# Kernel tuning notes

Hardware: AMD Instinct MI355X
Metric: run time of the kernel (lower is better)

## Reference

```python
import math
import jax, jax.numpy as jnp
import numpy as np

C = 256          # channels
HID = 64         # max(int(C*0.25),16)
RH = 64          # max(C//4,32) router hidden
N, S, H, W = 8, 64, 16, 16
LOW_FREQ_RATIO = 0.2
ROUTER_TEMP = 1.0
LN_EPS = 1e-5

def gelu(v):
    return jax.nn.gelu(v, approximate=False)

def bn1d(v, s, b):  # folded eval-mode BatchNorm1d: (N,C,S)
    return v * s[None, :, None] + b[None, :, None]

def conv1x1(v, w, b=None):  # v:(N,Cin,S), w:(Cout,Cin)
    o = jnp.einsum('oc,ncs->nos', w, v)
    if b is not None:
        o = o + b[None, :, None]
    return o

def convk(v, w):  # v:(N,Cin,S), w:(Cout,Cin,K), 'same' padding
    k = w.shape[-1]
    return jax.lax.conv_general_dilated(v, w, (1,), [(k // 2, k // 2)],
                                        dimension_numbers=('NCH', 'OIH', 'NCH'))

def setup_inputs():
    key = jax.random.key(0)
    ks = iter(jax.random.split(key, 64))
    def nrm(shape, sc=0.02):
        return jax.random.normal(next(ks), shape, jnp.float32) * sc
    d = {}
    d['x'] = jax.random.normal(next(ks), (N, C, S, H, W), jnp.float32)
    d['ln_g'] = jnp.ones((C,), jnp.float32)
    d['ln_b'] = jnp.zeros((C,), jnp.float32)
    for k in (3, 5, 7):
        d['mb_w%d' % k] = nrm((C, 3 * C, k))
        d['mb_s%d' % k] = 1.0 + nrm((C,))
        d['mb_b%d' % k] = nrm((C,))
    d['mf_w'] = nrm((C, C)); d['mf_s'] = 1.0 + nrm((C,)); d['mf_b'] = nrm((C,))
    d['pg_w1'] = nrm((HID, 3)); d['pg_s1'] = 1.0 + nrm((HID,)); d['pg_b1'] = nrm((HID,))
    d['pg_w2'] = nrm((C, HID)); d['pg_b2'] = nrm((C,))
    d['pp_w'] = nrm((C, C)); d['pp_s'] = 1.0 + nrm((C,)); d['pp_b'] = nrm((C,))
    d['mg_w'] = nrm((C, 2 * C)); d['mg_b'] = nrm((C,))
    d['mo_w1'] = nrm((C, 3 * C)); d['mo_s1'] = 1.0 + nrm((C,)); d['mo_b1'] = nrm((C,))
    d['mo_w2'] = nrm((C, C))
    d['rt_w1'] = nrm((RH, C + 5)); d['rt_b1'] = nrm((RH,))
    d['rt_w2'] = nrm((3, RH)); d['rt_b2'] = nrm((3,))
    d['bp_w1'] = nrm((C, 4 * C)); d['bp_s1'] = 1.0 + nrm((C,)); d['bp_b1'] = nrm((C,))
    d['bp_w2'] = nrm((C, C))
    d['res_scale'] = jnp.full((1, C, 1), 0.05, jnp.float32)
    d['fg_w'] = nrm((C, C)); d['fg_b'] = nrm((C,))
    d['sg_w'] = nrm((C, C)); d['sg_s'] = 1.0 + nrm((C,)); d['sg_b'] = nrm((C,))
    return d

def _forward(x, ln_g, ln_b, mb_w3, mb_s3, mb_b3, mb_w5, mb_s5, mb_b5,
             mb_w7, mb_s7, mb_b7, mf_w, mf_s, mf_b,
             pg_w1, pg_s1, pg_b1, pg_w2, pg_b2, pp_w, pp_s, pp_b,
             mg_w, mg_b, mo_w1, mo_s1, mo_b1, mo_w2,
             rt_w1, rt_b1, rt_w2, rt_b2, bp_w1, bp_s1, bp_b1, bp_w2,
             res_scale, fg_w, fg_b, sg_w, sg_s, sg_b):
    n, c, s = x.shape[:3]
    x32 = x.astype(jnp.float32)
    desc = x32.mean(axis=(-1, -2))                     # (N,C,S)
    t = desc.transpose(0, 2, 1)                        # (N,S,C)
    mu = t.mean(-1, keepdims=True)
    var = t.var(-1, keepdims=True)
    dn = (((t - mu) / jnp.sqrt(var + LN_EPS)) * ln_g + ln_b).transpose(0, 2, 1)  # (N,C,S)

    def tdiff(v, order):
        dd = v[:, :, order:] - v[:, :, :-order]
        return jnp.pad(dd, ((0, 0), (0, 0), (order, 0)))
    diff1 = tdiff(dn, 1)
    diff2 = tdiff(dn, 2)

    # motion branch (multi-kernel conv1d + BN + GELU)
    mi = jnp.concatenate([dn, diff1, diff2], axis=1)   # (N,3C,S)
    motion = 0.0
    for w, bs, bb in ((mb_w3, mb_s3, mb_b3), (mb_w5, mb_s5, mb_b5), (mb_w7, mb_s7, mb_b7)):
        motion = motion + gelu(bn1d(convk(mi, w), bs, bb))
    motion = gelu(bn1d(conv1x1(motion / 3.0, mf_w), mf_s, mf_b))

    # FFT-based cycle / phase estimation
    tokens = dn.transpose(0, 2, 1)                     # (N,S,C)
    freq = jnp.fft.rfft(tokens, axis=1, norm='ortho')  # (N,F,C) complex
    fe = jnp.abs(freq).mean(-1)                        # (N,F)
    Fb = fe.shape[1]
    low = min(max(int(round(Fb * LOW_FREQ_RATIO)), 1), Fb - 1)
    he = fe[:, low:]
    peak_rel = jnp.argmax(he, axis=-1)                 # (N,)
    peak_idx = peak_rel + low
    peak_val = jnp.take_along_axis(he, peak_rel[:, None], axis=1)
    cycle_conf = peak_val / jnp.maximum(he.sum(axis=1, keepdims=True), 1e-6)  # (N,1)
    peak_norm = peak_idx.astype(jnp.float32)[:, None] / float(Fb - 1)
    mean_freq = freq.mean(-1)                          # (N,F) complex
    dom = jnp.take_along_axis(mean_freq, peak_idx[:, None], axis=1)[:, 0]
    dom_phase = jnp.arctan2(dom.imag, dom.real)
    tax = jnp.arange(s, dtype=jnp.float32)
    ang = (2.0 * math.pi / max(s, 1)) * peak_idx.astype(jnp.float32)
    arg = ang[:, None] * tax[None, :] + dom_phase[:, None]
    phase_cos = jnp.cos(arg)[:, None, :]               # (N,1,S)
    phase_sin = jnp.sin(arg)[:, None, :]

    cycle_token = jnp.broadcast_to(cycle_conf[:, :, None], (n, 1, s))
    pf = jnp.concatenate([phase_cos, phase_sin, cycle_token], axis=1)  # (N,3,S)
    pgate = jax.nn.sigmoid(conv1x1(gelu(bn1d(conv1x1(pf, pg_w1), pg_s1, pg_b1)), pg_w2, pg_b2))
    phase = gelu(bn1d(conv1x1(dn * pgate, pp_w), pp_s, pp_b))

    # bidirectional EMA memory via lax.scan
    gate = jax.nn.sigmoid(conv1x1(jnp.concatenate([dn, jnp.abs(diff1)], axis=1), mg_w, mg_b))
    g = gate.transpose(2, 0, 1)                        # (S,N,C)
    dd = dn.transpose(2, 0, 1)
    def step(st, gd):
        gt, dt = gd
        st = gt * st + (1.0 - gt) * dt
        return st, st
    _, fo = jax.lax.scan(step, dd[0], (g[1:], dd[1:]))
    fwd_mem = jnp.concatenate([dd[:1], fo], axis=0).transpose(1, 2, 0)
    _, bo = jax.lax.scan(step, dd[-1], (g[-2::-1], dd[-2::-1]))
    bwd_mem = jnp.concatenate([dd[-1:], bo], axis=0)[::-1].transpose(1, 2, 0)
    memory = conv1x1(gelu(bn1d(conv1x1(
        jnp.concatenate([dn, fwd_mem, bwd_mem], axis=1), mo_w1), mo_s1, mo_b1)), mo_w2)

    # router
    seq_std = dn.std(axis=2).mean(axis=1, keepdims=True)
    diff_energy = jnp.abs(diff1).mean(axis=(1, 2))[:, None]
    motion_energy = jnp.abs(motion).mean(axis=(1, 2))[:, None]
    memory_energy = jnp.abs(memory - dn).mean(axis=(1, 2))[:, None]
    stats = jnp.concatenate([seq_std, diff_energy, cycle_conf, peak_norm,
                             memory_energy + motion_energy], axis=-1)
    ri = jnp.concatenate([dn.mean(-1), stats], axis=-1)  # (N,C+5)
    hdn = gelu(ri @ rt_w1.T + rt_b1)
    logits = hdn @ rt_w2.T + rt_b2
    bw = jax.nn.softmax(logits / max(ROUTER_TEMP, 1e-6), axis=-1)  # (N,3)
    fused = (bw[:, 0, None, None] * motion + bw[:, 1, None, None] * phase
             + bw[:, 2, None, None] * memory)

    delta = conv1x1(gelu(bn1d(conv1x1(
        jnp.concatenate([dn, fused, motion - phase, memory - dn], axis=1),
        bp_w1), bp_s1, bp_b1)), bp_w2)
    delta = delta * jax.nn.sigmoid(conv1x1(dn, fg_w, fg_b))
    delta = res_scale * delta
    delta = delta[:, :, :, None, None]                 # (N,C,S,1,1)

    sp = x32.mean(axis=2)                              # (N,C,H,W)
    sg_lin = jnp.einsum('oc,nchw->nohw', sg_w, sp)
    sgate = jax.nn.sigmoid(sg_lin * sg_s[None, :, None, None] + sg_b[None, :, None, None])
    delta = delta * sgate[:, :, None, :, :]            # (N,C,S,H,W)
    return x + delta.astype(x.dtype)

def reference(x, ln_g, ln_b, mb_w3, mb_s3, mb_b3, mb_w5, mb_s5, mb_b5,
              mb_w7, mb_s7, mb_b7, mf_w, mf_s, mf_b,
              pg_w1, pg_s1, pg_b1, pg_w2, pg_b2, pp_w, pp_s, pp_b,
              mg_w, mg_b, mo_w1, mo_s1, mo_b1, mo_w2,
              rt_w1, rt_b1, rt_w2, rt_b2, bp_w1, bp_s1, bp_b1, bp_w2,
              res_scale, fg_w, fg_b, sg_w, sg_s, sg_b):
    return _forward(x, ln_g, ln_b, mb_w3, mb_s3, mb_b3, mb_w5, mb_s5, mb_b5,
                    mb_w7, mb_s7, mb_b7, mf_w, mf_s, mf_b,
                    pg_w1, pg_s1, pg_b1, pg_w2, pg_b2, pp_w, pp_s, pp_b,
                    mg_w, mg_b, mo_w1, mo_s1, mo_b1, mo_w2,
                    rt_w1, rt_b1, rt_w2, rt_b2, bp_w1, bp_s1, bp_b1, bp_w2,
                    res_scale, fg_w, fg_b, sg_w, sg_s, sg_b)
```

## Files before the change

kernel.cpp:

```cpp
#include <hip/hip_runtime.h>
#include <math.h>

namespace {

constexpr int N_ = 8, C_ = 256, S_ = 64, HW_ = 256;
constexpr int NS = N_ * S_;
constexpr int NHW = N_ * HW_;

constexpr size_t O_DESC  = 0;
constexpr size_t O_DN    = 131072;
constexpr size_t O_MOT   = 393216;
constexpr size_t O_GATE  = 524288;
constexpr size_t O_MEM   = 786432;
constexpr size_t O_PHASE = 1048576;
constexpr size_t O_DELTA = 1441792;
constexpr size_t O_SCN   = 1572864;
constexpr size_t O_SPT   = 2752512;
constexpr size_t O_SGATE = 3276800;
constexpr size_t O_FE    = 3801088;
constexpr size_t O_MFRE  = 3801600;
constexpr size_t O_MFIM  = 3802112;
constexpr size_t O_BW    = 3802656;
constexpr size_t O_ATMF  = 3802688;
constexpr size_t O_ATMG  = 3868224;
constexpr size_t O_ATMO1 = 3999296;
constexpr size_t O_ATMO2 = 4195904;
constexpr size_t O_ATPP  = 4261440;
constexpr size_t O_ATBP1 = 4326976;
constexpr size_t O_ATBP2 = 4589120;
constexpr size_t O_ATFG  = 4654656;
constexpr size_t O_ATSG  = 4720192;
constexpr size_t O_WFRAG = 4785728;
constexpr size_t O_IM2   = 6850112;
constexpr size_t O_CONVC = 8226368;

typedef __attribute__((ext_vector_type(4))) float f32x4;
typedef __attribute__((ext_vector_type(8))) short s16x8;
typedef __attribute__((ext_vector_type(8))) unsigned short u16x8;

__device__ __forceinline__ float gelu_f(float v) {
  return 0.5f * v * (1.0f + erff(v * 0.70710678118654752f));
}
__device__ __forceinline__ float sigmoid_f(float v) {
  return 1.0f / (1.0f + expf(-v));
}
__device__ __forceinline__ unsigned short f2bf(float f) {
  unsigned int u = __float_as_uint(f);
  u += 0x7fffu + ((u >> 16) & 1u);
  return (unsigned short)(u >> 16);
}

__device__ __forceinline__ float block_sum256(float v, float* scratch) {
  #pragma unroll
  for (int off = 32; off; off >>= 1) v += __shfl_down(v, off, 64);
  int w = threadIdx.x >> 6;
  __syncthreads();
  if ((threadIdx.x & 63) == 0) scratch[w] = v;
  __syncthreads();
  return scratch[0] + scratch[1] + scratch[2] + scratch[3];
}

__device__ __forceinline__ void compute_pk(
    int n, const float* __restrict__ fe, const float* __restrict__ mfre,
    const float* __restrict__ mfim,
    float& conf, float& pnorm, float& dph, float& ang) {
  const float* f = fe + n * 33;
  float best = f[7]; int bidx = 0; float hs = 0.f;
  #pragma unroll
  for (int i = 0; i < 26; ++i) {
    float v = f[7 + i];
    hs += v;
    if (v > best) { best = v; bidx = i; }
  }
  int pi = bidx + 7;
  conf = best / fmaxf(hs, 1e-6f);
  pnorm = (float)pi * (1.f / 32.f);
  dph = atan2f(mfim[n * 33 + pi], mfre[n * 33 + pi]);
  ang = (6.283185307179586f / 64.f) * (float)pi;
}

__global__ __launch_bounds__(256) void weights_kernel(
    const float* __restrict__ wmf, const float* __restrict__ wmg,
    const float* __restrict__ wmo1, const float* __restrict__ wmo2,
    const float* __restrict__ wpp, const float* __restrict__ wbp1,
    const float* __restrict__ wbp2, const float* __restrict__ wfg,
    const float* __restrict__ wsg, float* __restrict__ ws,
    const float* __restrict__ w3, const float* __restrict__ w5,
    const float* __restrict__ w7, unsigned short* __restrict__ wf) {
  int bid = blockIdx.x;
  if (bid < 960) {
    __shared__ float tile[32][33];
    int xt = bid % 120, yt = bid / 120;
    const float* src; float* dst; int K;
    if      (xt < 8)   { src = wmf;  dst = ws + O_ATMF;  K = 256;  }
    else if (xt < 24)  { src = wmg;  dst = ws + O_ATMG;  K = 512;  xt -= 8;  }
    else if (xt < 48)  { src = wmo1; dst = ws + O_ATMO1; K = 768;  xt -= 24; }
    else if (xt < 56)  { src = wmo2; dst = ws + O_ATMO2; K = 256;  xt -= 48; }
    else if (xt < 64)  { src = wpp;  dst = ws + O_ATPP;  K = 256;  xt -= 56; }
    else if (xt < 96)  { src = wbp1; dst = ws + O_ATBP1; K = 1024; xt -= 64; }
    else if (xt < 104) { src = wbp2; dst = ws + O_ATBP2; K = 256;  xt -= 96; }
    else if (xt < 112) { src = wfg;  dst = ws + O_ATFG;  K = 256;  xt -= 104;}
    else               { src = wsg;  dst = ws + O_ATSG;  K = 256;  xt -= 112;}
    int tx = threadIdx.x & 31, ty = threadIdx.x >> 5;
    int c = xt * 32 + tx;
    #pragma unroll
    for (int i = 0; i < 4; ++i) {
      int r = yt * 32 + ty + i * 8;
      tile[ty + i * 8][tx] = src[(size_t)r * K + c];
    }
    __syncthreads();
    #pragma unroll
    for (int i = 0; i < 4; ++i) {
      int cc = xt * 32 + ty + i * 8;
      dst[(size_t)cc * 256 + yt * 32 + tx] = tile[tx][ty + i * 8];
    }
  } else {
    int g = (bid - 960) * 256 + threadIdx.x;
    int lane = g & 63;
    int m16 = (g >> 6) % 48;
    int kchunk = (g >> 6) / 48;
    int o = m16 * 16 + (lane & 15);
    int conv = o >> 8, oc = o & 255;
    int q = lane >> 4;
    u16x8 outv;
    #pragma unroll
    for (int j = 0; j < 8; ++j) {
      int k = kchunk * 32 + q * 8 + j;
      int ic = k / 7;
      int tau = k - ic * 7 - 3;
      float v = 0.f;
      if (conv == 0) {
        if (tau >= -1 && tau <= 1) v = w3[((size_t)oc * 768 + ic) * 3 + (tau + 1)];
      } else if (conv == 1) {
        if (tau >= -2 && tau <= 2) v = w5[((size_t)oc * 768 + ic) * 5 + (tau + 2)];
      } else {
        v = w7[((size_t)oc * 768 + ic) * 7 + (tau + 3)];
      }
      outv[j] = f2bf(v);
    }
    *((u16x8*)wf + g) = outv;
  }
}

__global__ __launch_bounds__(256) void reduce_x_kernel(
    const float* __restrict__ x, float* __restrict__ desc_t, float* __restrict__ sp_t) {
  int nc = blockIdx.x; int n = nc >> 8; int c = nc & 255;
  int t = threadIdx.x; int w = t >> 6; int l = t & 63;
  const float4* x4 = (const float4*)x + (size_t)nc * 4096;
  float4 sa = {0.f, 0.f, 0.f, 0.f};
  for (int i = 0; i < 16; ++i) {
    int s = w * 16 + i;
    float4 v = x4[(size_t)s * 64 + l];
    sa.x += v.x; sa.y += v.y; sa.z += v.z; sa.w += v.w;
    float ds = v.x + v.y + v.z + v.w;
    #pragma unroll
    for (int off = 32; off; off >>= 1) ds += __shfl_down(ds, off, 64);
    if (l == 0) desc_t[((size_t)n * 64 + s) * 256 + c] = ds * (1.f / 256.f);
  }
  __shared__ float4 lsp[4][64];
  lsp[w][l] = sa;
  __syncthreads();
  if (t < 64) {
    float4 a = lsp[0][t], b = lsp[1][t], c2 = lsp[2][t], d = lsp[3][t];
    float4 tot;
    tot.x = a.x + b.x + c2.x + d.x; tot.y = a.y + b.y + c2.y + d.y;
    tot.z = a.z + b.z + c2.z + d.z; tot.w = a.w + b.w + c2.w + d.w;
    size_t base = ((size_t)n * 256 + t * 4) * 256 + c;
    sp_t[base]       = tot.x * (1.f / 64.f);
    sp_t[base + 256] = tot.y * (1.f / 64.f);
    sp_t[base + 512] = tot.z * (1.f / 64.f);
    sp_t[base + 768] = tot.w * (1.f / 64.f);
  }
}

__global__ __launch_bounds__(256) void ln_kernel(
    const float* __restrict__ desc_t, const float* __restrict__ g,
    const float* __restrict__ b, float* __restrict__ dn_t) {
  __shared__ float sc[4];
  int col = blockIdx.x; int t = threadIdx.x;
  float v = desc_t[(size_t)col * 256 + t];
  float s1 = block_sum256(v, sc);
  float s2 = block_sum256(v * v, sc);
  float mu = s1 * (1.f / 256.f);
  float var = s2 * (1.f / 256.f) - mu * mu;
  float r = rsqrtf(var + 1e-5f);
  dn_t[(size_t)col * 256 + t] = (v - mu) * r * g[t] + b[t];
}

__global__ __launch_bounds__(256) void post_ln_kernel(
    const float* __restrict__ dn_t, const float* __restrict__ At_mg,
    const float* __restrict__ mg_b, float* __restrict__ gate_t,
    unsigned short* __restrict__ imf,
    float* __restrict__ fe, float* __restrict__ mfre, float* __restrict__ mfim) {
  __shared__ __align__(16) float smem[2048];
  int bid = blockIdx.x;
  int t = threadIdx.x;
  if (bid < 128) {
    int c0 = bid * 4;
    float4 f0, f1;
    {
      float d[4], a[4];
      #pragma unroll
      for (int i = 0; i < 4; ++i) {
        int col = c0 + i; int s = col & 63;
        float dd = dn_t[(size_t)col * 256 + t];
        float d1 = (s >= 1) ? dd - dn_t[(size_t)(col - 1) * 256 + t] : 0.f;
        d[i] = dd; a[i] = fabsf(d1);
      }
      f0.x = d[0]; f0.y = d[1]; f0.z = d[2]; f0.w = d[3];
      f1.x = a[0]; f1.y = a[1]; f1.z = a[2]; f1.w = a[3];
    }
    *(float4*)&smem[t * 4] = f0;
    *(float4*)&smem[(256 + t) * 4] = f1;
    __syncthreads();
    float a0 = 0.f, a1 = 0.f, a2 = 0.f, a3 = 0.f;
    #pragma unroll 4
    for (int k = 0; k < 512; ++k) {
      float a = At_mg[(size_t)k * 256 + t];
      float4 b = *(const float4*)&smem[k * 4];
      a0 += a * b.x; a1 += a * b.y; a2 += a * b.z; a3 += a * b.w;
    }
    float bb = mg_b[t];
    gate_t[(size_t)(c0 + 0) * 256 + t] = sigmoid_f(a0 + bb);
    gate_t[(size_t)(c0 + 1) * 256 + t] = sigmoid_f(a1 + bb);
    gate_t[(size_t)(c0 + 2) * 256 + t] = sigmoid_f(a2 + bb);
    gate_t[(size_t)(c0 + 3) * 256 + t] = sigmoid_f(a3 + bb);
  } else if (bid < 1472) {
    int g = (bid - 128) * 256 + t;
    int lane = g & 63;
    int c16 = (g >> 6) % 32;
    int kchunk = (g >> 6) / 32;
    int col = c16 * 16 + (lane & 15);
    int n = col >> 6, s = col & 63;
    int q = lane >> 4;
    const float* base = dn_t + (size_t)n * 16384;
    u16x8 outv;
    #pragma unroll
    for (int j = 0; j < 8; ++j) {
      int k = kchunk * 32 + q * 8 + j;
      int ic = k / 7;
      int tau = k - ic * 7 - 3;
      int stream = ic >> 8, c = ic & 255;
      int sp = s + tau;
      float v = 0.f;
      if (sp >= 0 && sp < 64) {
        float d = base[(size_t)sp * 256 + c];
        if (stream == 0) v = d;
        else if (stream == 1) v = (sp >= 1) ? d - base[(size_t)(sp - 1) * 256 + c] : 0.f;
        else v = (sp >= 2) ? d - base[(size_t)(sp - 2) * 256 + c] : 0.f;
      }
      outv[j] = f2bf(v);
    }
    *((u16x8*)imf + g) = outv;
  } else {
    int b = bid - 1472; int n = b / 33; int f = b % 33;
    float* cs = smem; float* sn = smem + 64; float* scr = smem + 128;
    if (t < 64) {
      int ft = (f * t) & 63;
      float ang = -6.283185307179586f * (float)ft * (1.f / 64.f);
      cs[t] = cosf(ang); sn[t] = sinf(ang);
    }
    __syncthreads();
    float re = 0.f, im = 0.f;
    const float* base = dn_t + (size_t)n * 16384 + t;
    for (int s = 0; s < 64; ++s) {
      float v = base[(size_t)s * 256];
      re += v * cs[s]; im += v * sn[s];
    }
    re *= 0.125f; im *= 0.125f;
    float mag = sqrtf(re * re + im * im);
    float sm = block_sum256(mag, scr);
    float sr = block_sum256(re, scr);
    float si = block_sum256(im, scr);
    if (t == 0) {
      fe[b]   = sm * (1.f / 256.f);
      mfre[b] = sr * (1.f / 256.f);
      mfim[b] = si * (1.f / 256.f);
    }
  }
}

__global__ __launch_bounds__(256) void conv_scan_kernel(
    const unsigned short* __restrict__ wf, const unsigned short* __restrict__ imf,
    float* __restrict__ partial,
    const float* __restrict__ dn_t, const float* __restrict__ gate_t,
    float* __restrict__ scn) {
  __shared__ float smem[16384];
  int bid = blockIdx.x;
  int t = threadIdx.x;
  if (bid < 384) {
    int mt = bid % 12; int rem = bid / 12;
    int nt = rem % 8; int kp = rem / 8;
    int lane = t & 63;
    int w = t >> 6;
    int m16 = mt * 4 + w;
    const s16x8* wfp = (const s16x8*)wf;
    const s16x8* imp = (const s16x8*)imf;
    f32x4 acc0 = {0.f,0.f,0.f,0.f}, acc1 = {0.f,0.f,0.f,0.f};
    f32x4 acc2 = {0.f,0.f,0.f,0.f}, acc3 = {0.f,0.f,0.f,0.f};
    #pragma unroll 2
    for (int cc = 0; cc < 42; ++cc) {
      int kc = kp * 42 + cc;
      s16x8 a = wfp[(size_t)(kc * 48 + m16) * 64 + lane];
      s16x8 b0 = imp[(size_t)(kc * 32 + nt * 4 + 0) * 64 + lane];
      s16x8 b1 = imp[(size_t)(kc * 32 + nt * 4 + 1) * 64 + lane];
      s16x8 b2 = imp[(size_t)(kc * 32 + nt * 4 + 2) * 64 + lane];
      s16x8 b3 = imp[(size_t)(kc * 32 + nt * 4 + 3) * 64 + lane];
      acc0 = __builtin_amdgcn_mfma_f32_16x16x32_bf16(a, b0, acc0, 0, 0, 0);
      acc1 = __builtin_amdgcn_mfma_f32_16x16x32_bf16(a, b1, acc1, 0, 0, 0);
      acc2 = __builtin_amdgcn_mfma_f32_16x16x32_bf16(a, b2, acc2, 0, 0, 0);
      acc3 = __builtin_amdgcn_mfma_f32_16x16x32_bf16(a, b3, acc3, 0, 0, 0);
    }
    int q = lane >> 4, ln = lane & 15;
    int o0 = m16 * 16 + q * 4;
    float* pb = partial + (size_t)kp * 393216;
    #pragma unroll
    for (int r = 0; r < 4; ++r) {
      size_t row = (size_t)(o0 + r) * 512;
      pb[row + (nt * 4 + 0) * 16 + ln] = acc0[r];
      pb[row + (nt * 4 + 1) * 16 + ln] = acc1[r];
      pb[row + (nt * 4 + 2) * 16 + ln] = acc2[r];
      pb[row + (nt * 4 + 3) * 16 + ln] = acc3[r];
    }
  } else {
    int idx = bid - 384;
    int n = idx >> 1, half = idx & 1;
    float* ld = smem;
    float* lg = smem + 8192;
    const float* dsrc = dn_t + (size_t)n * 16384 + half * 128;
    const float* gsrc = gate_t + (size_t)n * 16384 + half * 128;
    for (int i = t; i < 8192; i += 256) {
      int s = i >> 7, j = i & 127;
      ld[i] = dsrc[(size_t)s * 256 + j];
      lg[i] = gsrc[(size_t)s * 256 + j];
    }
    __syncthreads();
    int cl = t & 127;
    int c = half * 128 + cl;
    size_t ob = (size_t)n * 64 * 512 + c;
    if (t < 128) {
      float st = ld[cl];
      scn[ob] = st;
      for (int s = 1; s < 64; ++s) {
        float g = lg[s * 128 + cl], d = ld[s * 128 + cl];
        st = g * st + (1.f - g) * d;
        scn[ob + (size_t)s * 512] = st;
      }
    } else {
      float st = ld[63 * 128 + cl];
      scn[ob + (size_t)63 * 512 + 256] = st;
      for (int s = 62; s >= 0; --s) {
        float g = lg[s * 128 + cl], d = ld[s * 128 + cl];
        st = g * st + (1.f - g) * d;
        scn[ob + (size_t)s * 512 + 256] = st;
      }
    }
  }
}

__global__ __launch_bounds__(256) void mid_kernel(
    const float* __restrict__ P,
    const float* __restrict__ s3, const float* __restrict__ b3,
    const float* __restrict__ s5, const float* __restrict__ b5,
    const float* __restrict__ s7, const float* __restrict__ b7,
    const float* __restrict__ At_mf, const float* __restrict__ mf_s,
    const float* __restrict__ mf_b, float* __restrict__ motion_t,
    const float* __restrict__ dn_t, const float* __restrict__ scn,
    const float* __restrict__ At1, const float* __restrict__ sc1, const float* __restrict__ bi1,
    const float* __restrict__ At2, float* __restrict__ mem_t,
    const float* __restrict__ fe, const float* __restrict__ mfre, const float* __restrict__ mfim,
    const float* __restrict__ pg_w1, const float* __restrict__ pg_s1, const float* __restrict__ pg_b1,
    const float* __restrict__ pg_w2, const float* __restrict__ pg_b2,
    const float* __restrict__ At_pp, const float* __restrict__ pp_s, const float* __restrict__ pp_b,
    float* __restrict__ phase_t,
    const float* __restrict__ At_sg, const float* __restrict__ sp_t,
    const float* __restrict__ sg_s, const float* __restrict__ sg_b,
    float* __restrict__ sgate_t) {
  __shared__ __align__(16) float smem[4096];
  int bid = blockIdx.x;
  int t = threadIdx.x;
  if (bid < 128) {
    int c0 = bid * 4;
    float4 v3 = {0,0,0,0}, v5 = {0,0,0,0}, v7 = {0,0,0,0};
    #pragma unroll
    for (int kp = 0; kp < 4; ++kp) {
      const float* base = P + (size_t)kp * 393216 + c0;
      float4 x3 = *(const float4*)(base + (size_t)t * 512);
      float4 x5 = *(const float4*)(base + (size_t)(t + 256) * 512);
      float4 x7 = *(const float4*)(base + (size_t)(t + 512) * 512);
      v3.x += x3.x; v3.y += x3.y; v3.z += x3.z; v3.w += x3.w;
      v5.x += x5.x; v5.y += x5.y; v5.z += x5.z; v5.w += x5.w;
      v7.x += x7.x; v7.y += x7.y; v7.z += x7.z; v7.w += x7.w;
    }
    float s3v = s3[t], b3v = b3[t], s5v = s5[t], b5v = b5[t], s7v = s7[t], b7v = b7[t];
    float4 ms;
    ms.x = (gelu_f(v3.x*s3v+b3v) + gelu_f(v5.x*s5v+b5v) + gelu_f(v7.x*s7v+b7v)) * (1.f/3.f);
    ms.y = (gelu_f(v3.y*s3v+b3v) + gelu_f(v5.y*s5v+b5v) + gelu_f(v7.y*s7v+b7v)) * (1.f/3.f);
    ms.z = (gelu_f(v3.z*s3v+b3v) + gelu_f(v5.z*s5v+b5v) + gelu_f(v7.z*s7v+b7v)) * (1.f/3.f);
    ms.w = (gelu_f(v3.w*s3v+b3v) + gelu_f(v5.w*s5v+b5v) + gelu_f(v7.w*s7v+b7v)) * (1.f/3.f);
    *(float4*)&smem[t * 4] = ms;
    __syncthreads();
    float a0 = 0.f, a1 = 0.f, a2 = 0.f, a3 = 0.f;
    #pragma unroll 4
    for (int k = 0; k < 256; ++k) {
      float a = At_mf[(size_t)k * 256 + t];
      float4 b = *(const float4*)&smem[k * 4];
      a0 += a * b.x; a1 += a * b.y; a2 += a * b.z; a3 += a * b.w;
    }
    float sv = mf_s[t], bv2 = mf_b[t];
    motion_t[(size_t)(c0 + 0) * 256 + t] = gelu_f(a0 * sv + bv2);
    motion_t[(size_t)(c0 + 1) * 256 + t] = gelu_f(a1 * sv + bv2);
    motion_t[(size_t)(c0 + 2) * 256 + t] = gelu_f(a2 * sv + bv2);
    motion_t[(size_t)(c0 + 3) * 256 + t] = gelu_f(a3 * sv + bv2);
  } else if (bid < 256) {
    int c0 = (bid - 128) * 4;
    float* bv = smem;
    float* h4 = smem + 3072;
    float4 r0, r1, r2;
    #pragma unroll
    for (int i = 0; i < 4; ++i) {
      int col = c0 + i;
      ((float*)&r0)[i] = dn_t[(size_t)col * 256 + t];
      ((float*)&r1)[i] = scn[(size_t)col * 512 + t];
      ((float*)&r2)[i] = scn[(size_t)col * 512 + 256 + t];
    }
    *(float4*)&bv[t * 4] = r0;
    *(float4*)&bv[(256 + t) * 4] = r1;
    *(float4*)&bv[(512 + t) * 4] = r2;
    __syncthreads();
    float a0 = 0.f, a1 = 0.f, a2 = 0.f, a3 = 0.f;
    #pragma unroll 4
    for (int k = 0; k < 768; ++k) {
      float a = At1[(size_t)k * 256 + t];
      float4 b = *(const float4*)&bv[k * 4];
      a0 += a * b.x; a1 += a * b.y; a2 += a * b.z; a3 += a * b.w;
    }
    float sv = sc1[t], bb = bi1[t];
    float4 h;
    h.x = gelu_f(a0 * sv + bb); h.y = gelu_f(a1 * sv + bb);
    h.z = gelu_f(a2 * sv + bb); h.w = gelu_f(a3 * sv + bb);
    *(float4*)&h4[t * 4] = h;
    __syncthreads();
    float c0a = 0.f, c1a = 0.f, c2a = 0.f, c3a = 0.f;
    #pragma unroll 4
    for (int k = 0; k < 256; ++k) {
      float a = At2[(size_t)k * 256 + t];
      float4 b = *(const float4*)&h4[k * 4];
      c0a += a * b.x; c1a += a * b.y; c2a += a * b.z; c3a += a * b.w;
    }
    mem_t[(size_t)(c0 + 0) * 256 + t] = c0a;
    mem_t[(size_t)(c0 + 1) * 256 + t] = c1a;
    mem_t[(size_t)(c0 + 2) * 256 + t] = c2a;
    mem_t[(size_t)(c0 + 3) * 256 + t] = c3a;
  } else if (bid < 384) {
    int c0 = (bid - 256) * 4; int n = c0 >> 6; int s0 = c0 & 63;
    float* hh4 = smem;
    float* pin4 = smem + 256;
    float conf, pnorm, dph, ang;
    compute_pk(n, fe, mfre, mfim, conf, pnorm, dph, ang);
    (void)pnorm;
    if (t < 64) {
      float w0 = pg_w1[t * 3 + 0], w1 = pg_w1[t * 3 + 1], w2 = pg_w1[t * 3 + 2];
      float sv = pg_s1[t], bb = pg_b1[t];
      float4 hv;
      #pragma unroll
      for (int i = 0; i < 4; ++i) {
        float arg = ang * (float)(s0 + i) + dph;
        float v = w0 * cosf(arg) + w1 * sinf(arg) + w2 * conf;
        ((float*)&hv)[i] = gelu_f(v * sv + bb);
      }
      *(float4*)&hh4[t * 4] = hv;
    }
    __syncthreads();
    float p0, p1, p2, p3;
    {
      float bb = pg_b2[t];
      float a0 = bb, a1 = bb, a2 = bb, a3 = bb;
      const float* wrow = pg_w2 + t * 64;
      #pragma unroll 8
      for (int j = 0; j < 64; ++j) {
        float w = wrow[j];
        float4 h = *(const float4*)&hh4[j * 4];
        a0 += w * h.x; a1 += w * h.y; a2 += w * h.z; a3 += w * h.w;
      }
      p0 = sigmoid_f(a0); p1 = sigmoid_f(a1); p2 = sigmoid_f(a2); p3 = sigmoid_f(a3);
    }
    float4 pin;
    pin.x = dn_t[(size_t)(c0 + 0) * 256 + t] * p0;
    pin.y = dn_t[(size_t)(c0 + 1) * 256 + t] * p1;
    pin.z = dn_t[(size_t)(c0 + 2) * 256 + t] * p2;
    pin.w = dn_t[(size_t)(c0 + 3) * 256 + t] * p3;
    *(float4*)&pin4[t * 4] = pin;
    __syncthreads();
    float a0 = 0.f, a1 = 0.f, a2 = 0.f, a3 = 0.f;
    #pragma unroll 4
    for (int k = 0; k < 256; ++k) {
      float a = At_pp[(size_t)k * 256 + t];
      float4 b = *(const float4*)&pin4[k * 4];
      a0 += a * b.x; a1 += a * b.y; a2 += a * b.z; a3 += a * b.w;
    }
    float sv = pp_s[t], bb = pp_b[t];
    phase_t[(size_t)(c0 + 0) * 256 + t] = gelu_f(a0 * sv + bb);
    phase_t[(size_t)(c0 + 1) * 256 + t] = gelu_f(a1 * sv + bb);
    phase_t[(size_t)(c0 + 2) * 256 + t] = gelu_f(a2 * sv + bb);
    phase_t[(size_t)(c0 + 3) * 256 + t] = gelu_f(a3 * sv + bb);
  } else {
    int c0 = (bid - 384) * 4;
    float4 r0;
    #pragma unroll
    for (int i = 0; i < 4; ++i) {
      ((float*)&r0)[i] = sp_t[(size_t)(c0 + i) * 256 + t];
    }
    *(float4*)&smem[t * 4] = r0;
    __syncthreads();
    float a0 = 0.f, a1 = 0.f, a2 = 0.f, a3 = 0.f;
    #pragma unroll 4
    for (int k = 0; k < 256; ++k) {
      float a = At_sg[(size_t)k * 256 + t];
      float4 b = *(const float4*)&smem[k * 4];
      a0 += a * b.x; a1 += a * b.y; a2 += a * b.z; a3 += a * b.w;
    }
    float sv = sg_s[t], bb = sg_b[t];
    sgate_t[(size_t)(c0 + 0) * 256 + t] = sigmoid_f(a0 * sv + bb);
    sgate_t[(size_t)(c0 + 1) * 256 + t] = sigmoid_f(a1 * sv + bb);
    sgate_t[(size_t)(c0 + 2) * 256 + t] = sigmoid_f(a2 * sv + bb);
    sgate_t[(size_t)(c0 + 3) * 256 + t] = sigmoid_f(a3 * sv + bb);
  }
}

__global__ __launch_bounds__(256) void router_kernel(
    const float* __restrict__ dn_t, const float* __restrict__ motion_t,
    const float* __restrict__ memory_t,
    const float* __restrict__ fe, const float* __restrict__ mfre,
    const float* __restrict__ mfim,
    const float* __restrict__ rt_w1, const float* __restrict__ rt_b1,
    const float* __restrict__ rt_w2, const float* __restrict__ rt_b2,
    float* __restrict__ bw) {
  int n = blockIdx.x; int c = threadIdx.x;
  __shared__ float ri[261];
  __shared__ float h2[64];
  __shared__ float lg[3];
  __shared__ float sc[4];
  float sum = 0.f, sq = 0.f, ad1 = 0.f, amot = 0.f, amem = 0.f, prev = 0.f;
  for (int s = 0; s < 64; ++s) {
    size_t i = ((size_t)n * 64 + s) * 256 + c;
    float d = dn_t[i];
    sum += d; sq += d * d;
    if (s > 0) ad1 += fabsf(d - prev);
    prev = d;
    amot += fabsf(motion_t[i]);
    amem += fabsf(memory_t[i] - d);
  }
  float mean = sum * (1.f / 64.f);
  float var = sq * (1.f / 64.f) - mean * mean;
  float stdc = sqrtf(fmaxf(var, 0.f));
  ri[c] = mean;
  float rstd = block_sum256(stdc, sc);
  float rad1 = block_sum256(ad1, sc);
  float rmot = block_sum256(amot, sc);
  float rmem = block_sum256(amem, sc);
  if (c == 0) {
    float conf, pnorm, dph, ang;
    compute_pk(n, fe, mfre, mfim, conf, pnorm, dph, ang);
    (void)dph; (void)ang;
    ri[256] = rstd * (1.f / 256.f);
    ri[257] = rad1 * (1.f / 16384.f);
    ri[258] = conf;
    ri[259] = pnorm;
    ri[260] = (rmem + rmot) * (1.f / 16384.f);
  }
  __syncthreads();
  if (c < 64) {
    float acc = rt_b1[c];
    const float* wrow = rt_w1 + c * 261;
    for (int i = 0; i < 261; ++i) acc += wrow[i] * ri[i];
    h2[c] = gelu_f(acc);
  }
  __syncthreads();
  if (c < 3) {
    float acc = rt_b2[c];
    const float* wrow = rt_w2 + c * 64;
    #pragma unroll 8
    for (int j = 0; j < 64; ++j) acc += wrow[j] * h2[j];
    lg[c] = acc;
  }
  __syncthreads();
  if (c == 0) {
    float m = fmaxf(lg[0], fmaxf(lg[1], lg[2]));
    float e0 = expf(lg[0] - m), e1 = expf(lg[1] - m), e2 = expf(lg[2] - m);
    float inv = 1.f / (e0 + e1 + e2);
    bw[n * 3 + 0] = e0 * inv; bw[n * 3 + 1] = e1 * inv; bw[n * 3 + 2] = e2 * inv;
  }
}

__global__ __launch_bounds__(256) void delta_kernel(
    const float* __restrict__ dn_t, const float* __restrict__ motion_t,
    const float* __restrict__ phase_t, const float* __restrict__ mem_t,
    const float* __restrict__ bw,
    const float* __restrict__ At_fg, const float* __restrict__ fg_b,
    const float* __restrict__ At1, const float* __restrict__ sc1, const float* __restrict__ bi1,
    const float* __restrict__ At2, const float* __restrict__ rs,
    float* __restrict__ delta_t) {
  __shared__ __align__(16) float smem[5120];
  float* bv = smem;
  float* h4 = smem + 4096;
  int bid = blockIdx.x;
  int c0 = bid * 4; int n = c0 >> 6; int t = threadIdx.x;
  float w0 = bw[n * 3 + 0], w1 = bw[n * 3 + 1], w2 = bw[n * 3 + 2];
  float4 fd, ffu, fmp, fmd;
  #pragma unroll
  for (int i = 0; i < 4; ++i) {
    size_t idx = (size_t)(c0 + i) * 256 + t;
    float d = dn_t[idx], m = motion_t[idx], p = phase_t[idx], me = mem_t[idx];
    ((float*)&fd)[i] = d;
    ((float*)&ffu)[i] = w0 * m + w1 * p + w2 * me;
    ((float*)&fmp)[i] = m - p;
    ((float*)&fmd)[i] = me - d;
  }
  *(float4*)&bv[t * 4] = fd;
  *(float4*)&bv[(256 + t) * 4] = ffu;
  *(float4*)&bv[(512 + t) * 4] = fmp;
  *(float4*)&bv[(768 + t) * 4] = fmd;
  __syncthreads();
  float fg0, fg1, fg2, fg3;
  {
    float a0 = 0.f, a1 = 0.f, a2 = 0.f, a3 = 0.f;
    #pragma unroll 4
    for (int k = 0; k < 256; ++k) {
      float a = At_fg[(size_t)k * 256 + t];
      float4 b = *(const float4*)&bv[k * 4];
      a0 += a * b.x; a1 += a * b.y; a2 += a * b.z; a3 += a * b.w;
    }
    float bb = fg_b[t];
    fg0 = sigmoid_f(a0 + bb); fg1 = sigmoid_f(a1 + bb);
    fg2 = sigmoid_f(a2 + bb); fg3 = sigmoid_f(a3 + bb);
  }
  {
    float a0 = 0.f, a1 = 0.f, a2 = 0.f, a3 = 0.f;
    #pragma unroll 4
    for (int k = 0; k < 1024; ++k) {
      float a = At1[(size_t)k * 256 + t];
      float4 b = *(const float4*)&bv[k * 4];
      a0 += a * b.x; a1 += a * b.y; a2 += a * b.z; a3 += a * b.w;
    }
    float sv = sc1[t], bb = bi1[t];
    float4 h;
    h.x = gelu_f(a0 * sv + bb); h.y = gelu_f(a1 * sv + bb);
    h.z = gelu_f(a2 * sv + bb); h.w = gelu_f(a3 * sv + bb);
    *(float4*)&h4[t * 4] = h;
  }
  __syncthreads();
  float a0 = 0.f, a1 = 0.f, a2 = 0.f, a3 = 0.f;
  #pragma unroll 4
  for (int k = 0; k < 256; ++k) {
    float a = At2[(size_t)k * 256 + t];
    float4 b = *(const float4*)&h4[k * 4];
    a0 += a * b.x; a1 += a * b.y; a2 += a * b.z; a3 += a * b.w;
  }
  float rsv = rs[t];
  delta_t[(size_t)(c0 + 0) * 256 + t] = a0 * fg0 * rsv;
  delta_t[(size_t)(c0 + 1) * 256 + t] = a1 * fg1 * rsv;
  delta_t[(size_t)(c0 + 2) * 256 + t] = a2 * fg2 * rsv;
  delta_t[(size_t)(c0 + 3) * 256 + t] = a3 * fg3 * rsv;
}

__global__ __launch_bounds__(256) void final_kernel(
    const float* __restrict__ x, const float* __restrict__ delta_t,
    const float* __restrict__ sgate_t, float* __restrict__ out) {
  int nc = blockIdx.x; int n = nc >> 8; int c = nc & 255;
  int t = threadIdx.x;
  __shared__ float dlt[64];
  __shared__ float4 sgs4[64];
  if (t < 64) dlt[t] = delta_t[((size_t)n * 64 + t) * 256 + c];
  ((float*)sgs4)[t] = sgate_t[((size_t)n * 256 + t) * 256 + c];
  __syncthreads();
  const float4* x4 = (const float4*)x + (size_t)nc * 4096;
  float4* o4 = (float4*)out + (size_t)nc * 4096;
  int w = t >> 6, l = t & 63;
  float4 sg = sgs4[l];
  for (int i = 0; i < 16; ++i) {
    int s = w * 16 + i;
    float d = dlt[s];
    float4 v = x4[(size_t)s * 64 + l];
    v.x += d * sg.x; v.y += d * sg.y; v.z += d * sg.z; v.w += d * sg.w;
    o4[(size_t)s * 64 + l] = v;
  }
}

}

extern "C" void kernel_launch(void* const* d_in, const int* in_sizes, int n_in,
                              void* d_out, int out_size, void* d_ws, size_t ws_size,
                              hipStream_t stream) {
  const float* x      = (const float*)d_in[0];
  const float* ln_g   = (const float*)d_in[1];
  const float* ln_b   = (const float*)d_in[2];
  const float* mb_w3  = (const float*)d_in[3];
  const float* mb_s3  = (const float*)d_in[4];
  const float* mb_b3  = (const float*)d_in[5];
  const float* mb_w5  = (const float*)d_in[6];
  const float* mb_s5  = (const float*)d_in[7];
  const float* mb_b5  = (const float*)d_in[8];
  const float* mb_w7  = (const float*)d_in[9];
  const float* mb_s7  = (const float*)d_in[10];
  const float* mb_b7  = (const float*)d_in[11];
  const float* mf_w   = (const float*)d_in[12];
  const float* mf_s   = (const float*)d_in[13];
  const float* mf_b   = (const float*)d_in[14];
  const float* pg_w1  = (const float*)d_in[15];
  const float* pg_s1  = (const float*)d_in[16];
  const float* pg_b1  = (const float*)d_in[17];
  const float* pg_w2  = (const float*)d_in[18];
  const float* pg_b2  = (const float*)d_in[19];
  const float* pp_w   = (const float*)d_in[20];
  const float* pp_s   = (const float*)d_in[21];
  const float* pp_b   = (const float*)d_in[22];
  const float* mg_w   = (const float*)d_in[23];
  const float* mg_b   = (const float*)d_in[24];
  const float* mo_w1  = (const float*)d_in[25];
  const float* mo_s1  = (const float*)d_in[26];
  const float* mo_b1  = (const float*)d_in[27];
  const float* mo_w2  = (const float*)d_in[28];
  const float* rt_w1  = (const float*)d_in[29];
  const float* rt_b1  = (const float*)d_in[30];
  const float* rt_w2  = (const float*)d_in[31];
  const float* rt_b2  = (const float*)d_in[32];
  const float* bp_w1  = (const float*)d_in[33];
  const float* bp_s1  = (const float*)d_in[34];
  const float* bp_b1  = (const float*)d_in[35];
  const float* bp_w2  = (const float*)d_in[36];
  const float* res_sc = (const float*)d_in[37];
  const float* fg_w   = (const float*)d_in[38];
  const float* fg_b   = (const float*)d_in[39];
  const float* sg_w   = (const float*)d_in[40];
  const float* sg_s   = (const float*)d_in[41];
  const float* sg_b   = (const float*)d_in[42];
  float* ws = (float*)d_ws;
  float* out = (float*)d_out;
  unsigned short* wfrag = (unsigned short*)(ws + O_WFRAG);
  unsigned short* im2   = (unsigned short*)(ws + O_IM2);

  weights_kernel<<<2976, 256, 0, stream>>>(mf_w, mg_w, mo_w1, mo_w2, pp_w, bp_w1,
      bp_w2, fg_w, sg_w, ws, mb_w3, mb_w5, mb_w7, wfrag);
  reduce_x_kernel<<<2048, 256, 0, stream>>>(x, ws + O_DESC, ws + O_SPT);
  ln_kernel<<<512, 256, 0, stream>>>(ws + O_DESC, ln_g, ln_b, ws + O_DN);
  post_ln_kernel<<<1736, 256, 0, stream>>>(ws + O_DN, ws + O_ATMG, mg_b, ws + O_GATE,
      im2, ws + O_FE, ws + O_MFRE, ws + O_MFIM);
  conv_scan_kernel<<<400, 256, 0, stream>>>(wfrag, im2, ws + O_CONVC,
      ws + O_DN, ws + O_GATE, ws + O_SCN);
  mid_kernel<<<896, 256, 0, stream>>>(ws + O_CONVC, mb_s3, mb_b3, mb_s5, mb_b5,
      mb_s7, mb_b7, ws + O_ATMF, mf_s, mf_b, ws + O_MOT,
      ws + O_DN, ws + O_SCN, ws + O_ATMO1, mo_s1, mo_b1, ws + O_ATMO2, ws + O_MEM,
      ws + O_FE, ws + O_MFRE, ws + O_MFIM,
      pg_w1, pg_s1, pg_b1, pg_w2, pg_b2, ws + O_ATPP, pp_s, pp_b, ws + O_PHASE,
      ws + O_ATSG, ws + O_SPT, sg_s, sg_b, ws + O_SGATE);
  router_kernel<<<8, 256, 0, stream>>>(ws + O_DN, ws + O_MOT, ws + O_MEM,
      ws + O_FE, ws + O_MFRE, ws + O_MFIM, rt_w1, rt_b1, rt_w2, rt_b2, ws + O_BW);
  delta_kernel<<<128, 256, 0, stream>>>(ws + O_DN, ws + O_MOT, ws + O_PHASE, ws + O_MEM,
      ws + O_BW, ws + O_ATFG, fg_b, ws + O_ATBP1, bp_s1, bp_b1, ws + O_ATBP2, res_sc,
      ws + O_DELTA);
  final_kernel<<<2048, 256, 0, stream>>>(x, ws + O_DELTA, ws + O_SGATE, out);
}
```

Before: 638.2 us.

## Split delta kernel into one column per block with split-K partial sums

```diff
diff --git a/kernel.cpp b/kernel.cpp
--- a/kernel.cpp
+++ b/kernel.cpp
@@ -601,67 +601,77 @@
     const float* __restrict__ At1, const float* __restrict__ sc1, const float* __restrict__ bi1,
     const float* __restrict__ At2, const float* __restrict__ rs,
     float* __restrict__ delta_t) {
-  __shared__ __align__(16) float smem[5120];
-  float* bv = smem;
-  float* h4 = smem + 4096;
-  int bid = blockIdx.x;
-  int c0 = bid * 4; int n = c0 >> 6; int t = threadIdx.x;
+  __shared__ __align__(16) float bv[1024];
+  __shared__ __align__(16) float4 part[4][64];
+  __shared__ float hs[256];
+  __shared__ float fgs[256];
+  int col = blockIdx.x; int n = col >> 6; int t = threadIdx.x;
+  int w = t >> 6, ln = t & 63;
+  int oq = t >> 2, oc = t & 3;
   float w0 = bw[n * 3 + 0], w1 = bw[n * 3 + 1], w2 = bw[n * 3 + 2];
-  float4 fd, ffu, fmp, fmd;
-  #pragma unroll
-  for (int i = 0; i < 4; ++i) {
-    size_t idx = (size_t)(c0 + i) * 256 + t;
-    float d = dn_t[idx], m = motion_t[idx], p = phase_t[idx], me = mem_t[idx];
-    ((float*)&fd)[i] = d;
-    ((float*)&ffu)[i] = w0 * m + w1 * p + w2 * me;
-    ((float*)&fmp)[i] = m - p;
-    ((float*)&fmd)[i] = me - d;
-  }
-  *(float4*)&bv[t * 4] = fd;
-  *(float4*)&bv[(256 + t) * 4] = ffu;
-  *(float4*)&bv[(512 + t) * 4] = fmp;
-  *(float4*)&bv[(768 + t) * 4] = fmd;
-  __syncthreads();
-  float fg0, fg1, fg2, fg3;
+  size_t idx = (size_t)col * 256 + t;
+  float d = dn_t[idx], m = motion_t[idx], p = phase_t[idx], me = mem_t[idx];
+  bv[t]       = d;
+  bv[256 + t] = w0 * m + w1 * p + w2 * me;
+  bv[512 + t] = m - p;
+  bv[768 + t] = me - d;
+  __syncthreads();
   {
     float a0 = 0.f, a1 = 0.f, a2 = 0.f, a3 = 0.f;
-    #pragma unroll 4
-    for (int k = 0; k < 256; ++k) {
-      float a = At_fg[(size_t)k * 256 + t];
-      float4 b = *(const float4*)&bv[k * 4];
-      a0 += a * b.x; a1 += a * b.y; a2 += a * b.z; a3 += a * b.w;
-    }
-    float bb = fg_b[t];
-    fg0 = sigmoid_f(a0 + bb); fg1 = sigmoid_f(a1 + bb);
-    fg2 = sigmoid_f(a2 + bb); fg3 = sigmoid_f(a3 + bb);
-  }
+    int k0 = w * 64;
+    #pragma unroll 4
+    for (int k = k0; k < k0 + 64; ++k) {
+      float b = bv[k];
+      float4 a = *(const float4*)(At_fg + (size_t)k * 256 + ln * 4);
+      a0 += a.x * b; a1 += a.y * b; a2 += a.z * b; a3 += a.w * b;
+    }
+    float4 pr; pr.x = a0; pr.y = a1; pr.z = a2; pr.w = a3;
+    part[w][ln] = pr;
+  }
+  __syncthreads();
+  {
+    float r = ((const float*)&part[0][oq])[oc] + ((const float*)&part[1][oq])[oc]
+            + ((const float*)&part[2][oq])[oc] + ((const float*)&part[3][oq])[oc];
+    fgs[t] = sigmoid_f(r + fg_b[t]);
+  }
+  __syncthreads();
   {
     float a0 = 0.f, a1 = 0.f, a2 = 0.f, a3 = 0.f;
-    #pragma unroll 4
-    for (int k = 0; k < 1024; ++k) {
-      float a = At1[(size_t)k * 256 + t];
-      float4 b = *(const float4*)&bv[k * 4];
-      a0 += a * b.x; a1 += a * b.y; a2 += a * b.z; a3 += a * b.w;
-    }
-    float sv = sc1[t], bb = bi1[t];
-    float4 h;
-    h.x = gelu_f(a0 * sv + bb); h.y = gelu_f(a1 * sv + bb);
-    h.z = gelu_f(a2 * sv + bb); h.w = gelu_f(a3 * sv + bb);
-    *(float4*)&h4[t * 4] = h;
-  }
-  __syncthreads();
-  float a0 = 0.f, a1 = 0.f, a2 = 0.f, a3 = 0.f;
-  #pragma unroll 4
-  for (int k = 0; k < 256; ++k) {
-    float a = At2[(size_t)k * 256 + t];
-    float4 b = *(const float4*)&h4[k * 4];
-    a0 += a * b.x; a1 += a * b.y; a2 += a * b.z; a3 += a * b.w;
-  }
-  float rsv = rs[t];
-  delta_t[(size_t)(c0 + 0) * 256 + t] = a0 * fg0 * rsv;
-  delta_t[(size_t)(c0 + 1) * 256 + t] = a1 * fg1 * rsv;
-  delta_t[(size_t)(c0 + 2) * 256 + t] = a2 * fg2 * rsv;
-  delta_t[(size_t)(c0 + 3) * 256 + t] = a3 * fg3 * rsv;
+    int k0 = w * 256;
+    #pragma unroll 4
+    for (int k = k0; k < k0 + 256; ++k) {
+      float b = bv[k];
+      float4 a = *(const float4*)(At1 + (size_t)k * 256 + ln * 4);
+      a0 += a.x * b; a1 += a.y * b; a2 += a.z * b; a3 += a.w * b;
+    }
+    float4 pr; pr.x = a0; pr.y = a1; pr.z = a2; pr.w = a3;
+    part[w][ln] = pr;
+  }
+  __syncthreads();
+  {
+    float r = ((const float*)&part[0][oq])[oc] + ((const float*)&part[1][oq])[oc]
+            + ((const float*)&part[2][oq])[oc] + ((const float*)&part[3][oq])[oc];
+    hs[t] = gelu_f(r * sc1[t] + bi1[t]);
+  }
+  __syncthreads();
+  {
+    float a0 = 0.f, a1 = 0.f, a2 = 0.f, a3 = 0.f;
+    int k0 = w * 64;
+    #pragma unroll 4
+    for (int k = k0; k < k0 + 64; ++k) {
+      float b = hs[k];
+      float4 a = *(const float4*)(At2 + (size_t)k * 256 + ln * 4);
+      a0 += a.x * b; a1 += a.y * b; a2 += a.z * b; a3 += a.w * b;
+    }
+    float4 pr; pr.x = a0; pr.y = a1; pr.z = a2; pr.w = a3;
+    part[w][ln] = pr;
+  }
+  __syncthreads();
+  {
+    float r = ((const float*)&part[0][oq])[oc] + ((const float*)&part[1][oq])[oc]
+            + ((const float*)&part[2][oq])[oc] + ((const float*)&part[3][oq])[oc];
+    delta_t[idx] = r * fgs[t] * rs[t];
+  }
 }
 
 __global__ __launch_bounds__(256) void final_kernel(
@@ -756,7 +766,7 @@
       ws + O_ATSG, ws + O_SPT, sg_s, sg_b, ws + O_SGATE);
   router_kernel<<<8, 256, 0, stream>>>(ws + O_DN, ws + O_MOT, ws + O_MEM,
       ws + O_FE, ws + O_MFRE, ws + O_MFIM, rt_w1, rt_b1, rt_w2, rt_b2, ws + O_BW);
-  delta_kernel<<<128, 256, 0, stream>>>(ws + O_DN, ws + O_MOT, ws + O_PHASE, ws + O_MEM,
+  delta_kernel<<<512, 256, 0, stream>>>(ws + O_DN, ws + O_MOT, ws + O_PHASE, ws + O_MEM,
       ws + O_BW, ws + O_ATFG, fg_b, ws + O_ATBP1, bp_s1, bp_b1, ws + O_ATBP2, res_sc,
       ws + O_DELTA);
   final_kernel<<<2048, 256, 0, stream>>>(x, ws + O_DELTA, ws + O_SGATE, out);
```

New measurement: 564.4 us. 1.13x faster.
